# Optimization experiments

Measured on AMD Instinct MI355X. Metric: run time of the kernel, lower is better.

## Reference

```python
import jax, jax.numpy as jnp
import numpy as np

B, L, P, D = 512, 32, 256, 2


def hungarian(cost):
    """Min-cost assignment on an [n,n] numpy cost matrix (rows=pred, cols=target).
    Returns col[row]: target index assigned to each pred row (same as scipy
    linear_sum_assignment col_ind). Jonker-Volgenant style augmenting path."""
    n = cost.shape[0]
    INF = 1e18
    u = np.zeros(n + 1)
    v = np.zeros(n + 1)
    p = np.zeros(n + 1, dtype=np.int64)
    way = np.zeros(n + 1, dtype=np.int64)
    for i in range(1, n + 1):
        p[0] = i
        j0 = 0
        minv = np.full(n + 1, INF)
        used = np.zeros(n + 1, dtype=bool)
        while True:
            used[j0] = True
            i0 = p[j0]
            free = ~used[1:]
            cur = cost[i0 - 1, :] - u[i0] - v[1:]
            upd = free & (cur < minv[1:])
            m1 = minv[1:]
            m1[upd] = cur[upd]
            w1 = way[1:]
            w1[upd] = j0
            mfree = np.where(free, m1, INF)
            j1 = int(np.argmin(mfree)) + 1
            delta = mfree[j1 - 1]
            u[p[used]] += delta
            v[used] -= delta
            m1[free] -= delta
            j0 = j1
            if p[j0] == 0:
                break
        while j0:
            j1 = way[j0]
            p[j0] = p[j1]
            j0 = j1
    col = np.zeros(n, dtype=np.int64)
    for j in range(1, n + 1):
        col[p[j] - 1] = j - 1
    return col


def match_targets_np(pred_flat, tgt_flat, n_lines):
    """pred_flat/tgt_flat: np [B, L, P*D]; n_lines: np int [B].
    Replicates match_lines_sequence: Hungarian on pairwise squared L2 over the
    first n valid lines; unmatched rows stay zero (they are masked in the loss)."""
    out = np.zeros_like(pred_flat)
    for b in range(pred_flat.shape[0]):
        n = int(n_lines[b])
        if n == 1:
            out[b] = tgt_flat[b]
            continue
        pr = pred_flat[b, :n]
        tg = tgt_flat[b, :n]
        cost = ((pr[:, None, :] - tg[None, :, :]) ** 2).sum(-1)  # [pred, target]
        col = hungarian(cost)
        out[b, :n] = tgt_flat[b][col]
    return out


def setup_inputs() -> dict:
    key = jax.random.key(0)
    ks = jax.random.split(key, 5)
    point_pos_pred = jax.random.normal(ks[0], (B, L, P, D), jnp.float32)
    target_pos = jax.random.normal(ks[1], (B, L, P, D), jnp.float32)
    # probabilities in (0,1), bounded away from 0 so -log is finite
    line_prob_pred = jax.random.uniform(ks[2], (B, L, 2), jnp.float32) * 0.9 + 0.05
    n_lines = jax.random.randint(ks[3], (B,), 1, L + 1)
    line_masks = (jnp.arange(L)[None, :] < n_lines[:, None]).astype(jnp.float32)
    clf_line = jax.random.randint(ks[4], (B, L), 0, 2).astype(jnp.int32)
    point_masks = (line_masks[:, :, None] * jnp.ones((1, 1, P), jnp.float32))
    return {
        "point_pos_pred": point_pos_pred,
        "line_prob_pred": line_prob_pred,
        "target_pos": target_pos,
        "line_masks": line_masks,
        "clf_line": clf_line,
        "point_masks": point_masks,
    }


def reference(point_pos_pred, line_prob_pred, target_pos, line_masks, clf_line, point_masks):
    # --- Hungarian matching (host-side, non-differentiable, as in the original) ---
    pp = np.asarray(point_pos_pred).reshape(B, L, P * D)
    tp = np.asarray(target_pos).reshape(B, L, P * D)
    n_lines = np.asarray(line_masks).sum(axis=1).astype(np.int64)
    matched = jnp.asarray(match_targets_np(pp, tp, n_lines)).reshape(B, L, P, D)
    # --- masked MSE over (point, dim) ---
    sq = jnp.sum((point_pos_pred - matched) ** 2, axis=-1) * point_masks  # [B,L,P]
    mask_mse = jnp.sum(sq) / jnp.sum(point_masks)
    # --- masked NLL on line existence probabilities ---
    neg_log = -jnp.log(line_prob_pred).reshape(-1, 2)        # [B*L, 2]
    picked = jnp.take_along_axis(neg_log, clf_line.reshape(-1, 1), axis=1)
    clf_loss = jnp.sum(picked * line_masks.reshape(-1, 1)) / jnp.sum(line_masks)
    return (mask_mse, clf_loss)
```

## Files before the change

### kernel.cpp

```cpp
#include <hip/hip_runtime.h>
#include <cstdint>
#include <cstddef>

#define NB 512
#define NL 32
#define KD 512
#define KSLAB 128
#define PASS 128

__device__ __forceinline__ int swz128(int row, int ch) {
  int csw = (ch & ~15) | ((ch ^ (row >> 1)) & 15);
  return row * PASS + csw * 4;
}

__global__ __launch_bounds__(256, 2)
void cost_kernel(const float* __restrict__ pred, const float* __restrict__ tgt,
                 float* __restrict__ cost_part) {
  __shared__ float smem[8192];
  const int bid = blockIdx.x;
  const int b  = bid >> 2;
  const int ks = (bid & 3) * KSLAB;
  const int tid = threadIdx.x;
  float* predH = smem;
  float* tgtH  = smem + 4096;

  const int w = tid >> 6, l = tid & 63;
  const int ti = l >> 3, tj = l & 7;
  float acc[4][4];
#pragma unroll
  for (int a = 0; a < 4; ++a)
#pragma unroll
    for (int c2 = 0; c2 < 4; ++c2) acc[a][c2] = 0.f;

  const size_t base = (size_t)b * (NL * KD) + ks;
#pragma unroll
  for (int it = 0; it < 4; ++it) {
    int chunk = tid + it * 256;
    int row = chunk >> 5, ch = chunk & 31;
    const float4 pv = *reinterpret_cast<const float4*>(pred + base + (size_t)row * KD + ch * 4);
    const float4 tv = *reinterpret_cast<const float4*>(tgt  + base + (size_t)row * KD + ch * 4);
    int off = swz128(row, ch);
    *reinterpret_cast<float4*>(predH + off) = pv;
    *reinterpret_cast<float4*>(tgtH  + off) = tv;
  }
  __syncthreads();
#pragma unroll
  for (int c0 = 0; c0 < 8; ++c0) {
    const int c = (w << 3) + c0;
    float4 pr[4], tg[4];
#pragma unroll
    for (int r = 0; r < 4; ++r) {
      pr[r] = *reinterpret_cast<const float4*>(predH + swz128(4 * ti + r, c));
      tg[r] = *reinterpret_cast<const float4*>(tgtH  + swz128(4 * tj + r, c));
    }
#pragma unroll
    for (int a = 0; a < 4; ++a)
#pragma unroll
      for (int c2 = 0; c2 < 4; ++c2) {
        float d;
        d = pr[a].x - tg[c2].x; acc[a][c2] += d * d;
        d = pr[a].y - tg[c2].y; acc[a][c2] += d * d;
        d = pr[a].z - tg[c2].z; acc[a][c2] += d * d;
        d = pr[a].w - tg[c2].w; acc[a][c2] += d * d;
      }
  }
  __syncthreads();
#pragma unroll
  for (int a = 0; a < 4; ++a)
#pragma unroll
    for (int c2 = 0; c2 < 4; ++c2)
      smem[w * 1024 + (ti & 3) + 4 * tj + 32 * a + 128 * c2 + 512 * (ti >> 2)] = acc[a][c2];
  __syncthreads();
  const int ti2 = tid >> 5, a2 = (tid >> 3) & 3, tj2 = tid & 7;
  float ov[4];
#pragma unroll
  for (int k = 0; k < 4; ++k) {
    int ad = (ti2 & 3) + 4 * tj2 + 32 * a2 + 128 * k + 512 * (ti2 >> 2);
    ov[k] = (smem[ad] + smem[ad + 1024]) + (smem[ad + 2048] + smem[ad + 3072]);
  }
  *reinterpret_cast<float4*>(cost_part + (size_t)bid * 1024 + tid * 4) =
      make_float4(ov[0], ov[1], ov[2], ov[3]);
}

__device__ __forceinline__ float readlane_f(float x, int lane) {
  return __int_as_float(__builtin_amdgcn_readlane(__float_as_int(x), lane));
}
__device__ __forceinline__ int readlane_i(int x, int lane) {
  return __builtin_amdgcn_readlane(x, lane);
}

template<int CTRL, int RM>
__device__ __forceinline__ unsigned int dppumin(unsigned int x) {
  unsigned int m = (unsigned int)__builtin_amdgcn_update_dpp((int)x, (int)x, CTRL, RM, 0xf, false);
  return x < m ? x : m;
}
__device__ __forceinline__ unsigned int wave_umin32_bcast(unsigned int x) {
  x = dppumin<0xB1, 0xf>(x);
  x = dppumin<0x4E, 0xf>(x);
  x = dppumin<0x124, 0xf>(x);
  x = dppumin<0x128, 0xf>(x);
  x = dppumin<0x142, 0xa>(x);
  return (unsigned int)__builtin_amdgcn_readlane((int)x, 31);
}

__global__ __launch_bounds__(64)
void hung_kernel(const float* __restrict__ cost_part,
                 const float* __restrict__ prob,
                 const float* __restrict__ lmask,
                 const int* __restrict__ clf,
                 float* __restrict__ part) {
  __shared__ float cs[1024];
  const int b = blockIdx.x;
  const int lane = threadIdx.x;

  {
    const float4* p0 = reinterpret_cast<const float4*>(cost_part + (size_t)(4 * b + 0) * 1024);
    const float4* p1 = reinterpret_cast<const float4*>(cost_part + (size_t)(4 * b + 1) * 1024);
    const float4* p2 = reinterpret_cast<const float4*>(cost_part + (size_t)(4 * b + 2) * 1024);
    const float4* p3 = reinterpret_cast<const float4*>(cost_part + (size_t)(4 * b + 3) * 1024);
    float4* cs4 = reinterpret_cast<float4*>(cs);
#pragma unroll
    for (int k = 0; k < 4; ++k) {
      int i = lane + 64 * k;
      float4 x0 = p0[i], x1 = p1[i], x2 = p2[i], x3 = p3[i];
      cs4[i] = make_float4((x0.x + x1.x) + (x2.x + x3.x),
                           (x0.y + x1.y) + (x2.y + x3.y),
                           (x0.z + x1.z) + (x2.z + x3.z),
                           (x0.w + x1.w) + (x2.w + x3.w));
    }
  }

  float lm = (lane < 32) ? lmask[b * 32 + lane] : 0.f;
  const int n = __popcll(__ballot(lm > 0.5f));
  float clfpart = 0.f;
  if (lane < 32 && lm > 0.5f) {
    int cc = clf[b * 32 + lane];
    clfpart = -logf(prob[(size_t)(b * 32 + lane) * 2 + cc]);
  }
  __syncthreads();

  const float FINF = 1e30f;
  const bool activecol = (lane < n);
  const int cl = lane & 31;

  float u_r = 0.f, v_j = 0.f;
  int p_j = -1;

  for (int ri = 0; ri < n; ++ri) {
    int i0 = ri;
    bool usedc = false;
    bool usedr = (lane == ri);
    float rowv = cs[i0 * 32 + cl];
    float u0 = readlane_f(u_r, i0);
    while (true) {
      float key = rowv - v_j;
      bool act = activecol && !usedc;
      float m = act ? key : FINF;
      unsigned int mu = __float_as_uint(m);
      mu ^= (unsigned int)((int)mu >> 31) | 0x80000000u;
      unsigned int packed = (mu & 0xFFFFFFE0u) | (unsigned int)cl;
      unsigned int pmin = wave_umin32_bcast(packed);
      int j1 = (int)(pmin & 31u);
      float mnv = readlane_f(m, j1);
      int pj1 = readlane_i(p_j, j1);
      float delta = mnv - u0;
      if (usedr) u_r += delta;
      if (usedc) v_j -= delta;
      if (pj1 < 0) {
        if (lane == j1) p_j = ri;
        break;
      }
      usedc = usedc || (lane == j1);
      usedr = usedr || (lane == pj1);
      i0 = pj1;
      rowv = cs[i0 * 32 + cl];
      u0 = readlane_f(u_r, i0);
    }
  }

  int pj = p_j < 0 ? 0 : p_j;
  float a = activecol ? cs[pj * 32 + cl] : 0.f;
#pragma unroll
  for (int off = 32; off; off >>= 1) {
    a += __shfl_xor(a, off);
    clfpart += __shfl_xor(clfpart, off);
  }
  if (lane == 0) {
    part[b * 3 + 0] = a;
    part[b * 3 + 1] = clfpart;
    part[b * 3 + 2] = (float)n;
  }
}

__global__ void finalize_kernel(const float* __restrict__ part, float* __restrict__ out) {
  const int lane = threadIdx.x;
  double cs = 0.0, ls = 0.0, ns = 0.0;
  for (int i = lane; i < NB; i += 64) {
    cs += (double)part[i * 3 + 0];
    ls += (double)part[i * 3 + 1];
    ns += (double)part[i * 3 + 2];
  }
#pragma unroll
  for (int off = 32; off; off >>= 1) {
    cs += __shfl_xor(cs, off);
    ls += __shfl_xor(ls, off);
    ns += __shfl_xor(ns, off);
  }
  if (lane == 0) {
    out[0] = (float)(cs / (ns * 256.0));
    out[1] = (float)(ls / ns);
  }
}

extern "C" void kernel_launch(void* const* d_in, const int* in_sizes, int n_in,
                              void* d_out, int out_size, void* d_ws, size_t ws_size,
                              hipStream_t stream) {
  const float* pred = (const float*)d_in[0];
  const float* prob = (const float*)d_in[1];
  const float* tgt  = (const float*)d_in[2];
  const float* lm   = (const float*)d_in[3];
  const int*   clf  = (const int*)d_in[4];

  float* cost_part = (float*)d_ws;
  float* part = cost_part + (size_t)2048 * 1024;

  cost_kernel<<<NB * 4, 256, 0, stream>>>(pred, tgt, cost_part);
  hung_kernel<<<NB, 64, 0, stream>>>(cost_part, prob, lm, clf, part);
  finalize_kernel<<<1, 64, 0, stream>>>(part, (float*)d_out);
}
```

Measured before the change: 59.37 us.

## Fuse finalize into Hungarian kernel via last-block atomic; shrink cost blocks

The finalize launch is removed. The last Hungarian block to finish, detected with an atomic counter and a threadfence, now performs the global reduction. A memset is added to reset the counter on every call. The cost kernel now uses 128-thread blocks that stage two 64-wide half-slabs in half the shared memory, which lowers LDS use per block but adds an extra sync round per block.

```diff
diff --git a/kernel.cpp b/kernel.cpp
--- a/kernel.cpp
+++ b/kernel.cpp
@@ -6,23 +6,23 @@
 #define NL 32
 #define KD 512
 #define KSLAB 128
-#define PASS 128
-
-__device__ __forceinline__ int swz128(int row, int ch) {
-  int csw = (ch & ~15) | ((ch ^ (row >> 1)) & 15);
+#define PASS 64
+
+__device__ __forceinline__ int swz64(int row, int ch) {
+  int csw = (ch ^ (row >> 1)) & 15;
   return row * PASS + csw * 4;
 }
 
-__global__ __launch_bounds__(256, 2)
+__global__ __launch_bounds__(128, 2)
 void cost_kernel(const float* __restrict__ pred, const float* __restrict__ tgt,
                  float* __restrict__ cost_part) {
-  __shared__ float smem[8192];
+  __shared__ float smem[4096];
   const int bid = blockIdx.x;
   const int b  = bid >> 2;
   const int ks = (bid & 3) * KSLAB;
   const int tid = threadIdx.x;
   float* predH = smem;
-  float* tgtH  = smem + 4096;
+  float* tgtH  = smem + 2048;
 
   const int w = tid >> 6, l = tid & 63;
   const int ti = l >> 3, tj = l & 7;
@@ -32,37 +32,40 @@
 #pragma unroll
     for (int c2 = 0; c2 < 4; ++c2) acc[a][c2] = 0.f;
 
-  const size_t base = (size_t)b * (NL * KD) + ks;
-#pragma unroll
-  for (int it = 0; it < 4; ++it) {
-    int chunk = tid + it * 256;
-    int row = chunk >> 5, ch = chunk & 31;
-    const float4 pv = *reinterpret_cast<const float4*>(pred + base + (size_t)row * KD + ch * 4);
-    const float4 tv = *reinterpret_cast<const float4*>(tgt  + base + (size_t)row * KD + ch * 4);
-    int off = swz128(row, ch);
-    *reinterpret_cast<float4*>(predH + off) = pv;
-    *reinterpret_cast<float4*>(tgtH  + off) = tv;
-  }
-  __syncthreads();
-#pragma unroll
-  for (int c0 = 0; c0 < 8; ++c0) {
-    const int c = (w << 3) + c0;
-    float4 pr[4], tg[4];
-#pragma unroll
-    for (int r = 0; r < 4; ++r) {
-      pr[r] = *reinterpret_cast<const float4*>(predH + swz128(4 * ti + r, c));
-      tg[r] = *reinterpret_cast<const float4*>(tgtH  + swz128(4 * tj + r, c));
-    }
-#pragma unroll
-    for (int a = 0; a < 4; ++a)
-#pragma unroll
-      for (int c2 = 0; c2 < 4; ++c2) {
-        float d;
-        d = pr[a].x - tg[c2].x; acc[a][c2] += d * d;
-        d = pr[a].y - tg[c2].y; acc[a][c2] += d * d;
-        d = pr[a].z - tg[c2].z; acc[a][c2] += d * d;
-        d = pr[a].w - tg[c2].w; acc[a][c2] += d * d;
+  for (int hp = 0; hp < 2; ++hp) {
+    __syncthreads();
+    const size_t base = (size_t)b * (NL * KD) + ks + hp * PASS;
+#pragma unroll
+    for (int it = 0; it < 4; ++it) {
+      int chunk = tid + it * 128;
+      int row = chunk >> 4, ch = chunk & 15;
+      const float4 pv = *reinterpret_cast<const float4*>(pred + base + (size_t)row * KD + ch * 4);
+      const float4 tv = *reinterpret_cast<const float4*>(tgt  + base + (size_t)row * KD + ch * 4);
+      int off = swz64(row, ch);
+      *reinterpret_cast<float4*>(predH + off) = pv;
+      *reinterpret_cast<float4*>(tgtH  + off) = tv;
+    }
+    __syncthreads();
+#pragma unroll
+    for (int c0 = 0; c0 < 8; ++c0) {
+      const int c = (w << 3) + c0;
+      float4 pr[4], tg[4];
+#pragma unroll
+      for (int r = 0; r < 4; ++r) {
+        pr[r] = *reinterpret_cast<const float4*>(predH + swz64(4 * ti + r, c));
+        tg[r] = *reinterpret_cast<const float4*>(tgtH  + swz64(4 * tj + r, c));
       }
+#pragma unroll
+      for (int a = 0; a < 4; ++a)
+#pragma unroll
+        for (int c2 = 0; c2 < 4; ++c2) {
+          float d;
+          d = pr[a].x - tg[c2].x; acc[a][c2] += d * d;
+          d = pr[a].y - tg[c2].y; acc[a][c2] += d * d;
+          d = pr[a].z - tg[c2].z; acc[a][c2] += d * d;
+          d = pr[a].w - tg[c2].w; acc[a][c2] += d * d;
+        }
+    }
   }
   __syncthreads();
 #pragma unroll
@@ -71,15 +74,18 @@
     for (int c2 = 0; c2 < 4; ++c2)
       smem[w * 1024 + (ti & 3) + 4 * tj + 32 * a + 128 * c2 + 512 * (ti >> 2)] = acc[a][c2];
   __syncthreads();
-  const int ti2 = tid >> 5, a2 = (tid >> 3) & 3, tj2 = tid & 7;
-  float ov[4];
-#pragma unroll
-  for (int k = 0; k < 4; ++k) {
-    int ad = (ti2 & 3) + 4 * tj2 + 32 * a2 + 128 * k + 512 * (ti2 >> 2);
-    ov[k] = (smem[ad] + smem[ad + 1024]) + (smem[ad + 2048] + smem[ad + 3072]);
-  }
-  *reinterpret_cast<float4*>(cost_part + (size_t)bid * 1024 + tid * 4) =
-      make_float4(ov[0], ov[1], ov[2], ov[3]);
+  const int i = tid >> 2, j0 = (tid & 3) * 8;
+  const int ti3 = i >> 2;
+  float ov[8];
+#pragma unroll
+  for (int kk = 0; kk < 8; ++kk) {
+    int j = j0 + kk;
+    int ad = (ti3 & 3) + 4 * (j >> 2) + 32 * (i & 3) + 128 * (j & 3) + 512 * (ti3 >> 2);
+    ov[kk] = smem[ad] + smem[ad + 1024];
+  }
+  float* dst = cost_part + (size_t)bid * 1024 + i * 32 + j0;
+  *reinterpret_cast<float4*>(dst)     = make_float4(ov[0], ov[1], ov[2], ov[3]);
+  *reinterpret_cast<float4*>(dst + 4) = make_float4(ov[4], ov[5], ov[6], ov[7]);
 }
 
 __device__ __forceinline__ float readlane_f(float x, int lane) {
@@ -108,7 +114,9 @@
                  const float* __restrict__ prob,
                  const float* __restrict__ lmask,
                  const int* __restrict__ clf,
-                 float* __restrict__ part) {
+                 float* __restrict__ part,
+                 unsigned int* __restrict__ counter,
+                 float* __restrict__ out) {
   __shared__ float cs[1024];
   const int b = blockIdx.x;
   const int lane = threadIdx.x;
@@ -190,25 +198,30 @@
     part[b * 3 + 1] = clfpart;
     part[b * 3 + 2] = (float)n;
   }
-}
-
-__global__ void finalize_kernel(const float* __restrict__ part, float* __restrict__ out) {
-  const int lane = threadIdx.x;
-  double cs = 0.0, ls = 0.0, ns = 0.0;
-  for (int i = lane; i < NB; i += 64) {
-    cs += (double)part[i * 3 + 0];
-    ls += (double)part[i * 3 + 1];
-    ns += (double)part[i * 3 + 2];
-  }
-#pragma unroll
-  for (int off = 32; off; off >>= 1) {
-    cs += __shfl_xor(cs, off);
-    ls += __shfl_xor(ls, off);
-    ns += __shfl_xor(ns, off);
-  }
-  if (lane == 0) {
-    out[0] = (float)(cs / (ns * 256.0));
-    out[1] = (float)(ls / ns);
+
+  __threadfence();
+  unsigned int t = 0;
+  if (lane == 0) t = atomicAdd(counter, 1u);
+  t = (unsigned int)__shfl((int)t, 0);
+  if (t == NB - 1u) {
+    __threadfence();
+    volatile const float* vp = part;
+    double csum = 0.0, lsum = 0.0, nsum = 0.0;
+    for (int i = lane; i < NB; i += 64) {
+      csum += (double)vp[i * 3 + 0];
+      lsum += (double)vp[i * 3 + 1];
+      nsum += (double)vp[i * 3 + 2];
+    }
+#pragma unroll
+    for (int off = 32; off; off >>= 1) {
+      csum += __shfl_xor(csum, off);
+      lsum += __shfl_xor(lsum, off);
+      nsum += __shfl_xor(nsum, off);
+    }
+    if (lane == 0) {
+      out[0] = (float)(csum / (nsum * 256.0));
+      out[1] = (float)(lsum / nsum);
+    }
   }
 }
 
@@ -223,8 +236,10 @@
 
   float* cost_part = (float*)d_ws;
   float* part = cost_part + (size_t)2048 * 1024;
-
-  cost_kernel<<<NB * 4, 256, 0, stream>>>(pred, tgt, cost_part);
-  hung_kernel<<<NB, 64, 0, stream>>>(cost_part, prob, lm, clf, part);
-  finalize_kernel<<<1, 64, 0, stream>>>(part, (float*)d_out);
-}
+  unsigned int* counter = (unsigned int*)(part + NB * 3);
+
+  hipMemsetAsync(counter, 0, sizeof(unsigned int), stream);
+  cost_kernel<<<NB * 4, 128, 0, stream>>>(pred, tgt, cost_part);
+  hung_kernel<<<NB, 64, 0, stream>>>(cost_part, prob, lm, clf, part, counter,
+                                     (float*)d_out);
+}
```

After: 73.03 us. 23.0% more time.

## Shorten Hungarian loop reduction latency and fuse finalize into last block

Applied to the files above, without the earlier changes.

The wave-wide argmin now ends with a ds_swizzle xor-16 step instead of a row_bcast plus readlane, so every lane holds the minimum without going through a scalar broadcast. The min value is decoded from the packed key, and the next row's cost is prefetched from shared memory before the branch. The separate finalize kernel is replaced by a last-block-done atomic counter inside hung_kernel, which removes one launch but adds a memset launch and a global atomic.

```diff
diff --git a/kernel.cpp b/kernel.cpp
--- a/kernel.cpp
+++ b/kernel.cpp
@@ -82,25 +82,23 @@
       make_float4(ov[0], ov[1], ov[2], ov[3]);
 }
 
-__device__ __forceinline__ float readlane_f(float x, int lane) {
-  return __int_as_float(__builtin_amdgcn_readlane(__float_as_int(x), lane));
-}
-__device__ __forceinline__ int readlane_i(int x, int lane) {
-  return __builtin_amdgcn_readlane(x, lane);
-}
-
 template<int CTRL, int RM>
 __device__ __forceinline__ unsigned int dppumin(unsigned int x) {
   unsigned int m = (unsigned int)__builtin_amdgcn_update_dpp((int)x, (int)x, CTRL, RM, 0xf, false);
   return x < m ? x : m;
 }
-__device__ __forceinline__ unsigned int wave_umin32_bcast(unsigned int x) {
-  x = dppumin<0xB1, 0xf>(x);
-  x = dppumin<0x4E, 0xf>(x);
-  x = dppumin<0x124, 0xf>(x);
-  x = dppumin<0x128, 0xf>(x);
-  x = dppumin<0x142, 0xa>(x);
-  return (unsigned int)__builtin_amdgcn_readlane((int)x, 31);
+__device__ __forceinline__ unsigned int swz_xor16(unsigned int x) {
+  return (unsigned int)__builtin_amdgcn_ds_swizzle((int)x, 0x401F);
+}
+__device__ __forceinline__ int bperm_i(int x, int srclane) {
+  return __builtin_amdgcn_ds_bpermute(srclane << 2, x);
+}
+__device__ __forceinline__ float bperm_f(float x, int srclane) {
+  return __int_as_float(__builtin_amdgcn_ds_bpermute(srclane << 2, __float_as_int(x)));
+}
+__device__ __forceinline__ float unsort_f(unsigned int y) {
+  unsigned int x = (y & 0x80000000u) ? (y ^ 0x80000000u) : ~y;
+  return __uint_as_float(x);
 }
 
 __global__ __launch_bounds__(64)
@@ -108,10 +106,13 @@
                  const float* __restrict__ prob,
                  const float* __restrict__ lmask,
                  const int* __restrict__ clf,
-                 float* __restrict__ part) {
+                 float* __restrict__ part,
+                 unsigned int* __restrict__ counter,
+                 float* __restrict__ out) {
   __shared__ float cs[1024];
   const int b = blockIdx.x;
   const int lane = threadIdx.x;
+  const int cl = lane & 31;
 
   {
     const float4* p0 = reinterpret_cast<const float4*>(cost_part + (size_t)(4 * b + 0) * 1024);
@@ -140,8 +141,7 @@
   __syncthreads();
 
   const float FINF = 1e30f;
-  const bool activecol = (lane < n);
-  const int cl = lane & 31;
+  const bool activecol = (cl < n);
 
   float u_r = 0.f, v_j = 0.f;
   int p_j = -1;
@@ -149,37 +149,42 @@
   for (int ri = 0; ri < n; ++ri) {
     int i0 = ri;
     bool usedc = false;
-    bool usedr = (lane == ri);
+    bool usedr = (cl == ri);
     float rowv = cs[i0 * 32 + cl];
-    float u0 = readlane_f(u_r, i0);
+    float u0 = bperm_f(u_r, i0);
     while (true) {
       float key = rowv - v_j;
-      bool act = activecol && !usedc;
-      float m = act ? key : FINF;
+      float m = (activecol && !usedc) ? key : FINF;
       unsigned int mu = __float_as_uint(m);
       mu ^= (unsigned int)((int)mu >> 31) | 0x80000000u;
       unsigned int packed = (mu & 0xFFFFFFE0u) | (unsigned int)cl;
-      unsigned int pmin = wave_umin32_bcast(packed);
-      int j1 = (int)(pmin & 31u);
-      float mnv = readlane_f(m, j1);
-      int pj1 = readlane_i(p_j, j1);
+      packed = dppumin<0xB1, 0xf>(packed);
+      packed = dppumin<0x4E, 0xf>(packed);
+      packed = dppumin<0x124, 0xf>(packed);
+      packed = dppumin<0x128, 0xf>(packed);
+      { unsigned int o = swz_xor16(packed); packed = packed < o ? packed : o; }
+      int j1 = (int)(packed & 31u);
+      int pj1 = bperm_i(p_j, j1);
+      int i0n = pj1 < 0 ? 0 : pj1;
+      float rowv_n = cs[i0n * 32 + cl];
+      float mnv = unsort_f(packed & 0xFFFFFFE0u);
       float delta = mnv - u0;
       if (usedr) u_r += delta;
       if (usedc) v_j -= delta;
       if (pj1 < 0) {
-        if (lane == j1) p_j = ri;
+        if (cl == j1) p_j = ri;
         break;
       }
-      usedc = usedc || (lane == j1);
-      usedr = usedr || (lane == pj1);
-      i0 = pj1;
-      rowv = cs[i0 * 32 + cl];
-      u0 = readlane_f(u_r, i0);
+      usedc = usedc || (cl == j1);
+      usedr = usedr || (cl == pj1);
+      i0 = i0n;
+      rowv = rowv_n;
+      u0 = bperm_f(u_r, i0n);
     }
   }
 
   int pj = p_j < 0 ? 0 : p_j;
-  float a = activecol ? cs[pj * 32 + cl] : 0.f;
+  float a = (lane < n) ? cs[pj * 32 + cl] : 0.f;
 #pragma unroll
   for (int off = 32; off; off >>= 1) {
     a += __shfl_xor(a, off);
@@ -190,25 +195,30 @@
     part[b * 3 + 1] = clfpart;
     part[b * 3 + 2] = (float)n;
   }
-}
-
-__global__ void finalize_kernel(const float* __restrict__ part, float* __restrict__ out) {
-  const int lane = threadIdx.x;
-  double cs = 0.0, ls = 0.0, ns = 0.0;
-  for (int i = lane; i < NB; i += 64) {
-    cs += (double)part[i * 3 + 0];
-    ls += (double)part[i * 3 + 1];
-    ns += (double)part[i * 3 + 2];
-  }
-#pragma unroll
-  for (int off = 32; off; off >>= 1) {
-    cs += __shfl_xor(cs, off);
-    ls += __shfl_xor(ls, off);
-    ns += __shfl_xor(ns, off);
-  }
-  if (lane == 0) {
-    out[0] = (float)(cs / (ns * 256.0));
-    out[1] = (float)(ls / ns);
+
+  __threadfence();
+  unsigned int t = 0;
+  if (lane == 0) t = atomicAdd(counter, 1u);
+  t = (unsigned int)__shfl((int)t, 0);
+  if (t == NB - 1u) {
+    __threadfence();
+    volatile const float* vp = part;
+    double csum = 0.0, lsum = 0.0, nsum = 0.0;
+    for (int i = lane; i < NB; i += 64) {
+      csum += (double)vp[i * 3 + 0];
+      lsum += (double)vp[i * 3 + 1];
+      nsum += (double)vp[i * 3 + 2];
+    }
+#pragma unroll
+    for (int off = 32; off; off >>= 1) {
+      csum += __shfl_xor(csum, off);
+      lsum += __shfl_xor(lsum, off);
+      nsum += __shfl_xor(nsum, off);
+    }
+    if (lane == 0) {
+      out[0] = (float)(csum / (nsum * 256.0));
+      out[1] = (float)(lsum / nsum);
+    }
   }
 }
 
@@ -223,8 +233,10 @@
 
   float* cost_part = (float*)d_ws;
   float* part = cost_part + (size_t)2048 * 1024;
-
+  unsigned int* counter = (unsigned int*)(part + NB * 3);
+
+  hipMemsetAsync(counter, 0, sizeof(unsigned int), stream);
   cost_kernel<<<NB * 4, 256, 0, stream>>>(pred, tgt, cost_part);
-  hung_kernel<<<NB, 64, 0, stream>>>(cost_part, prob, lm, clf, part);
-  finalize_kernel<<<1, 64, 0, stream>>>(part, (float*)d_out);
-}
+  hung_kernel<<<NB, 64, 0, stream>>>(cost_part, prob, lm, clf, part, counter,
+                                     (float*)d_out);
+}
```

Measured after the change: 70.14 us. 1.18x slower.
